# Kernel optimization log

Hardware: AMD Instinct MI355X
Metric: run time of the kernel (lower is better)

## Reference

```python
import jax, jax.numpy as jnp
import numpy as np

EPS = 1e-12  # F.normalize eps


def _gather_nb(var, idx):
    # var: [B, N, C], idx: [B, N, K] -> [B, N, K, C]; out[b,n,k,c] = var[b, idx[b,n,k], c]
    return jnp.take_along_axis(var[:, :, None, :], idx[:, :, :, None], axis=1)


def _l2norm(v):
    n = jnp.sqrt(jnp.sum(v * v, axis=-1, keepdims=True))
    return v / jnp.maximum(n, EPS)


def setup_inputs() -> dict:
    key = jax.random.key(0)
    ks = jax.random.split(key, 16)
    B, N, K, dim, hid = 4, 4096, 16, 128, 64
    s = 0.05
    return {
        "pos": jax.random.normal(ks[0], (B, N, 3), jnp.float32),
        "x": jax.random.normal(ks[1], (B, dim, N), jnp.float32),
        "idx": jax.random.randint(ks[2], (B, N, K), 0, N, jnp.int64),
        "dist": jax.random.uniform(ks[3], (B, N, K), jnp.float32),
        "W_qkv": jax.random.normal(ks[4], (3 * dim, dim), jnp.float32) * s,
        "W1": jax.random.normal(ks[5], (hid, 10), jnp.float32) * s,
        "b1": jax.random.normal(ks[6], (hid,), jnp.float32) * s,
        "W2": jax.random.normal(ks[7], (dim, hid), jnp.float32) * s,
        "b2": jax.random.normal(ks[8], (dim,), jnp.float32) * s,
        "Wm1": jax.random.normal(ks[9], (4 * dim, dim), jnp.float32) * s,
        "bm1": jax.random.normal(ks[10], (4 * dim,), jnp.float32) * s,
        "Wm2": jax.random.normal(ks[11], (dim, 4 * dim), jnp.float32) * s,
        "bm2": jax.random.normal(ks[12], (dim,), jnp.float32) * s,
    }


def reference(pos, x, idx, dist, W_qkv, W1, b1, W2, b2, Wm1, bm1, Wm2, bm2):
    B, _, N = x.shape
    xt = jnp.transpose(x, (0, 2, 1))                      # [B, N, C]
    qkv = xt @ W_qkv.T                                    # [B, N, 3C]
    Q, K_, V = jnp.split(qkv, 3, axis=-1)

    Qg = _gather_nb(Q, idx)                               # [B, N, K, C]
    Kg = _gather_nb(K_, idx)
    Vg = _gather_nb(V, idx)

    # position embedding: [center(3) | neighbor(3) | diff(3) | dist(1)] -> MLP 10->hid->C
    pos_nb = _gather_nb(pos, idx)                         # [B, N, K, 3]
    pos_c = jnp.broadcast_to(pos[:, :, None, :], pos_nb.shape)
    feat10 = jnp.concatenate(
        [pos_c, pos_nb, pos_c - pos_nb, dist[..., None]], axis=-1)  # [B, N, K, 10]
    pos_emb = jax.nn.relu(feat10 @ W1.T + b1) @ W2.T + b2  # [B, N, K, C]

    Knorm = _l2norm(Kg + pos_emb)                         # [B, N, K, C]
    Vrel = jax.nn.relu(Vg + pos_emb)                      # [B, N, K, C]
    Qn = _l2norm(Qg)                                      # [B, N, K, C]

    # kv_context: contract over N per neighbor slot k -> [B, K, C, C]
    kv = jnp.einsum('bnkc,bnkd->bkcd', Knorm, Vrel)
    # (1/N) Qn @ kv, then sum over k -> [B, N, C]
    agg = jnp.einsum('bnkc,bkcd->bnd', Qn, kv) / N

    out = jax.nn.relu(agg @ Wm1.T + bm1) @ Wm2.T + bm2 + xt  # [B, N, C]
    return jnp.transpose(out, (0, 2, 1))                     # [B, C, N]
```

## Files before the change

kernel.cpp:

```cpp
#include <hip/hip_runtime.h>
#include <math.h>

#define Bn 4
#define Nn 4096
#define Kn 16
#define Cn 128
#define HIDn 64

#define OFF_WQKVBF 0
#define OFF_WM1BF  24576
#define OFF_WM2BF  57344
#define OFF_W2BFG  90112
#define OFF_QNBF   94208
#define OFF_KMBF   1142784
#define OFF_VMBF   2191360
#define OFF_KVT32  3239936
#define OFF_KVTBF  4288512
#define OFF_AGG0   4812800
#define OFF_AGG1   6909952
#define OFF_FLAG   9007104

typedef short bf16x8 __attribute__((ext_vector_type(8)));
typedef float f32x4 __attribute__((ext_vector_type(4)));

__device__ inline unsigned short f2bf(float f) {
  union { float f; unsigned u; } v; v.f = f;
  unsigned r = v.u + 0x7fffu + ((v.u >> 16) & 1u);
  return (unsigned short)(r >> 16);
}
__device__ inline float b2f(unsigned short s) {
  union { unsigned u; float f; } v; v.u = ((unsigned)s) << 16; return v.f;
}

__global__ void k0_prep(const float* __restrict__ Wqkv,
                        const float* __restrict__ Wm1, const float* __restrict__ Wm2,
                        const float* __restrict__ W2,
                        const int* __restrict__ idx_raw, float* ws) {
  if (blockIdx.x == 0 && threadIdx.x == 0) {
    int any = 0;
    for (int i = 0; i < 64; ++i) any |= idx_raw[2 * i + 1];
    ((int*)(ws + OFF_FLAG))[0] = (any == 0) ? 1 : 0;
  }
  int t = blockIdx.x * 256 + threadIdx.x;
  if (t < 49152) { ((unsigned short*)(ws + OFF_WQKVBF))[t] = f2bf(Wqkv[t]); return; }
  t -= 49152;
  if (t < 65536) { ((unsigned short*)(ws + OFF_WM1BF))[t] = f2bf(Wm1[t]); return; }
  t -= 65536;
  if (t < 65536) { ((unsigned short*)(ws + OFF_WM2BF))[t] = f2bf(Wm2[t]); return; }
  t -= 65536;
  if (t < 8192) { ((unsigned short*)(ws + OFF_W2BFG))[t] = f2bf(W2[t]); return; }
}

__global__ __launch_bounds__(256, 2) void k1_qkv(const float* __restrict__ x, float* ws) {
  __shared__ __align__(16) unsigned short a_lds[32 * 136];
  __shared__ __align__(16) float qkv_lds[32 * 388];
  const unsigned short* Wq = (const unsigned short*)(ws + OFF_WQKVBF);
  unsigned short* Qnbf = (unsigned short*)(ws + OFF_QNBF);
  unsigned short* KmBF = (unsigned short*)(ws + OFF_KMBF);
  unsigned short* VmBF = (unsigned short*)(ws + OFF_VMBF);
  int b = blockIdx.x >> 7;
  int n0 = (blockIdx.x & 127) << 5;
  int t = threadIdx.x;
  int w = t >> 6, l = t & 63, ml = l & 15, gq = l >> 4;
#pragma unroll
  for (int i = 0; i < 16; ++i) {
    int id = t + 256 * i;
    int c = id >> 5, j = id & 31;
    a_lds[j * 136 + c] = f2bf(x[(b * Cn + c) * Nn + n0 + j]);
  }
  __syncthreads();
  f32x4 acc[2][6];
#pragma unroll
  for (int i = 0; i < 2; ++i)
#pragma unroll
    for (int j = 0; j < 6; ++j) acc[i][j] = (f32x4)0.f;
#pragma unroll
  for (int kc = 0; kc < 4; ++kc) {
    bf16x8 av0 = *(const bf16x8*)&a_lds[ml * 136 + kc * 32 + 8 * gq];
    bf16x8 av1 = *(const bf16x8*)&a_lds[(ml + 16) * 136 + kc * 32 + 8 * gq];
#pragma unroll
    for (int nf = 0; nf < 6; ++nf) {
      int m = 96 * w + 16 * nf + ml;
      bf16x8 bv = *(const bf16x8*)&Wq[m * 128 + kc * 32 + 8 * gq];
      acc[0][nf] = __builtin_amdgcn_mfma_f32_16x16x32_bf16(av0, bv, acc[0][nf], 0, 0, 0);
      acc[1][nf] = __builtin_amdgcn_mfma_f32_16x16x32_bf16(av1, bv, acc[1][nf], 0, 0, 0);
    }
  }
#pragma unroll
  for (int mf = 0; mf < 2; ++mf)
#pragma unroll
    for (int nf = 0; nf < 6; ++nf)
#pragma unroll
      for (int r = 0; r < 4; ++r)
        qkv_lds[(16 * mf + 4 * gq + r) * 388 + 96 * w + 16 * nf + ml] = acc[mf][nf][r];
  __syncthreads();
  {
    int g = t >> 3, l8 = t & 7;
    float4 q4[4];
    float ss = 0.f;
#pragma unroll
    for (int q = 0; q < 4; ++q) {
      q4[q] = *(const float4*)&qkv_lds[g * 388 + l8 * 16 + 4 * q];
      ss = fmaf(q4[q].x, q4[q].x, ss); ss = fmaf(q4[q].y, q4[q].y, ss);
      ss = fmaf(q4[q].z, q4[q].z, ss); ss = fmaf(q4[q].w, q4[q].w, ss);
    }
    ss += __shfl_xor(ss, 1); ss += __shfl_xor(ss, 2); ss += __shfl_xor(ss, 4);
    float sc = 1.f / fmaxf(sqrtf(ss), 1e-12f);
    union { unsigned short us[8]; uint4 u4; } o0, o1;
#pragma unroll
    for (int q = 0; q < 2; ++q) {
      o0.us[q * 4 + 0] = f2bf(q4[q].x * sc); o0.us[q * 4 + 1] = f2bf(q4[q].y * sc);
      o0.us[q * 4 + 2] = f2bf(q4[q].z * sc); o0.us[q * 4 + 3] = f2bf(q4[q].w * sc);
    }
#pragma unroll
    for (int q = 0; q < 2; ++q) {
      o1.us[q * 4 + 0] = f2bf(q4[2 + q].x * sc); o1.us[q * 4 + 1] = f2bf(q4[2 + q].y * sc);
      o1.us[q * 4 + 2] = f2bf(q4[2 + q].z * sc); o1.us[q * 4 + 3] = f2bf(q4[2 + q].w * sc);
    }
    *(uint4*)&Qnbf[(b * Nn + n0 + g) * Cn + l8 * 16] = o0.u4;
    *(uint4*)&Qnbf[(b * Nn + n0 + g) * Cn + l8 * 16 + 8] = o1.u4;
  }
#pragma unroll
  for (int i = 0; i < 2; ++i) {
    int id = t + 256 * i;
    int row = id >> 4, c8 = id & 15;
    const float* kp = &qkv_lds[row * 388 + 128 + c8 * 8];
    const float* vp = &qkv_lds[row * 388 + 256 + c8 * 8];
    union { unsigned short us[8]; uint4 u4; } ko, vo;
#pragma unroll
    for (int j = 0; j < 8; ++j) { ko.us[j] = f2bf(kp[j]); vo.us[j] = f2bf(vp[j]); }
    *(uint4*)&KmBF[(b * Nn + n0 + row) * Cn + c8 * 8] = ko.u4;
    *(uint4*)&VmBF[(b * Nn + n0 + row) * Cn + c8 * 8] = vo.u4;
  }
}

#define CH2 8
__global__ __launch_bounds__(256, 2) void k2_kv(const float* __restrict__ pos,
                                                const float* __restrict__ dist,
                                                const int* __restrict__ idxp,
                                                const float* __restrict__ W1,
                                                const float* __restrict__ b1,
                                                const float* __restrict__ b2,
                                                float* ws) {
  __shared__ __align__(16) unsigned short h_lds[32 * 72];
  __shared__ float pe_lds[32 * 132];
  __shared__ __align__(16) unsigned short KnT[128 * 40];
  __shared__ __align__(16) unsigned short VrT[128 * 40];
  __shared__ float W1s[640];
  __shared__ float b1s[64];
  __shared__ float b2s[128];
  __shared__ int jn_s[32];

  const unsigned short* KmBF = (const unsigned short*)(ws + OFF_KMBF);
  const unsigned short* VmBF = (const unsigned short*)(ws + OFF_VMBF);
  const unsigned short* W2g = (const unsigned short*)(ws + OFF_W2BFG);
  float* kvt = ws + OFF_KVT32;
  int flag = ((const int*)(ws + OFF_FLAG))[0];

  int bid = blockIdx.x;
  int b = bid & 3;
  int rest = bid >> 2;
  int k = rest & 15, ch = rest >> 4;
  int t = threadIdx.x;
  int w = t >> 6, l = t & 63;
  int ml = l & 15, gq = l >> 4;

  for (int i = t; i < 640; i += 256) W1s[i] = W1[i];
  if (t < 64) b1s[t] = b1[t];
  if (t < 128) b2s[t] = b2[t];

  f32x4 acc[2][8];
#pragma unroll
  for (int i = 0; i < 2; ++i)
#pragma unroll
    for (int j = 0; j < 8; ++j) acc[i][j] = (f32x4)0.f;

  int g = t >> 3, l8 = t & 7;

  for (int it = 0; it < 16; ++it) {
    int n0 = ch * 512 + it * 32;
    __syncthreads();
    {
      int n = n0 + g;
      int fidx = (b * Nn + n) * Kn + k;
      int jn = flag ? idxp[2 * fidx] : idxp[fidx];
      if (l8 == 0) jn_s[g] = jn;
      float dd = dist[fidx];
      float pc0 = pos[(b * Nn + n) * 3 + 0], pc1 = pos[(b * Nn + n) * 3 + 1], pc2 = pos[(b * Nn + n) * 3 + 2];
      float pn0 = pos[(b * Nn + jn) * 3 + 0], pn1 = pos[(b * Nn + jn) * 3 + 1], pn2 = pos[(b * Nn + jn) * 3 + 2];
      float f10[10] = {pc0, pc1, pc2, pn0, pn1, pn2, pc0 - pn0, pc1 - pn1, pc2 - pn2, dd};
      union { unsigned short us[8]; uint4 u4; } hv;
#pragma unroll
      for (int oo = 0; oo < 8; ++oo) {
        int o = l8 * 8 + oo;
        float a = b1s[o];
#pragma unroll
        for (int i2 = 0; i2 < 10; ++i2) a = fmaf(W1s[o * 10 + i2], f10[i2], a);
        hv.us[oo] = f2bf(fmaxf(a, 0.f));
      }
      *(uint4*)&h_lds[g * 72 + l8 * 8] = hv.u4;
    }
    __syncthreads();
    {
      f32x4 pacc[2][2];
#pragma unroll
      for (int i = 0; i < 2; ++i)
#pragma unroll
        for (int j = 0; j < 2; ++j) pacc[i][j] = (f32x4)0.f;
#pragma unroll
      for (int hc = 0; hc < 64; hc += 32) {
        bf16x8 av[2];
#pragma unroll
        for (int mf = 0; mf < 2; ++mf)
          av[mf] = *(const bf16x8*)&h_lds[(ml + 16 * mf) * 72 + hc + 8 * gq];
#pragma unroll
        for (int nf = 0; nf < 2; ++nf) {
          int c = 32 * w + 16 * nf + ml;
          bf16x8 bv = *(const bf16x8*)&W2g[c * 64 + hc + 8 * gq];
          pacc[0][nf] = __builtin_amdgcn_mfma_f32_16x16x32_bf16(av[0], bv, pacc[0][nf], 0, 0, 0);
          pacc[1][nf] = __builtin_amdgcn_mfma_f32_16x16x32_bf16(av[1], bv, pacc[1][nf], 0, 0, 0);
        }
      }
#pragma unroll
      for (int mf = 0; mf < 2; ++mf)
#pragma unroll
        for (int nf = 0; nf < 2; ++nf) {
          int c = 32 * w + 16 * nf + ml;
          float b2v = b2s[c];
#pragma unroll
          for (int r = 0; r < 4; ++r)
            pe_lds[(16 * mf + 4 * gq + r) * 132 + c] = pacc[mf][nf][r] + b2v;
        }
    }
    __syncthreads();
    {
      int jn = jn_s[g];
      const unsigned short* krow = &KmBF[(b * Nn + jn) * Cn];
      const unsigned short* vrow = &VmBF[(b * Nn + jn) * Cn];
      union { unsigned short us[8]; uint4 u4; } ka, kb, va, vb;
      ka.u4 = *(const uint4*)&krow[l8 * 16];
      kb.u4 = *(const uint4*)&krow[l8 * 16 + 8];
      va.u4 = *(const uint4*)&vrow[l8 * 16];
      vb.u4 = *(const uint4*)&vrow[l8 * 16 + 8];
      float kr[16], vr[16];
      float ss = 0.f;
#pragma unroll
      for (int q = 0; q < 4; ++q) {
        float4 p = *(const float4*)&pe_lds[g * 132 + l8 * 16 + 4 * q];
        float pv[4] = {p.x, p.y, p.z, p.w};
#pragma unroll
        for (int j2 = 0; j2 < 4; ++j2) {
          int j = 4 * q + j2;
          unsigned short ku = (j < 8) ? ka.us[j] : kb.us[j - 8];
          unsigned short vu = (j < 8) ? va.us[j] : vb.us[j - 8];
          kr[j] = b2f(ku) + pv[j2];
          vr[j] = fmaxf(b2f(vu) + pv[j2], 0.f);
          ss = fmaf(kr[j], kr[j], ss);
        }
      }
      ss += __shfl_xor(ss, 1); ss += __shfl_xor(ss, 2); ss += __shfl_xor(ss, 4);
      float sc = 1.f / fmaxf(sqrtf(ss), 1e-12f);
#pragma unroll
      for (int j = 0; j < 16; ++j) {
        int c = l8 * 16 + j;
        int sw = g ^ (((c >> 4) & 3) << 3);
        KnT[c * 40 + sw] = f2bf(kr[j] * sc);
        VrT[c * 40 + sw] = f2bf(vr[j]);
      }
    }
    __syncthreads();
    {
      bf16x8 av[2];
#pragma unroll
      for (int mf = 0; mf < 2; ++mf) {
        int d = 32 * w + 16 * mf + ml;
        av[mf] = *(const bf16x8*)&VrT[d * 40 + (8 * gq ^ ((((d >> 4) & 3)) << 3))];
      }
#pragma unroll
      for (int nf = 0; nf < 8; ++nf) {
        int c = 16 * nf + ml;
        bf16x8 bv = *(const bf16x8*)&KnT[c * 40 + (8 * gq ^ ((((c >> 4) & 3)) << 3))];
#pragma unroll
        for (int mf = 0; mf < 2; ++mf)
          acc[mf][nf] = __builtin_amdgcn_mfma_f32_16x16x32_bf16(av[mf], bv, acc[mf][nf], 0, 0, 0);
      }
    }
  }
  float* kvp = kvt + (b * Kn + k) * Cn * Cn;
#pragma unroll
  for (int mf = 0; mf < 2; ++mf)
#pragma unroll
    for (int nf = 0; nf < 8; ++nf) {
      int c = 16 * nf + ml;
#pragma unroll
      for (int r = 0; r < 4; ++r) {
        int d = 32 * w + 16 * mf + 4 * gq + r;
        atomicAdd(&kvp[d * Cn + c], acc[mf][nf][r]);
      }
    }
}

__global__ __launch_bounds__(256) void k2b_cvt(float* ws) {
  const float* src = ws + OFF_KVT32;
  unsigned short* dst = (unsigned short*)(ws + OFF_KVTBF);
  int i = blockIdx.x * 256 + threadIdx.x;
  float4 a = *(const float4*)&src[i * 8];
  float4 c = *(const float4*)&src[i * 8 + 4];
  union { unsigned short us[8]; uint4 u4; } o;
  o.us[0] = f2bf(a.x); o.us[1] = f2bf(a.y); o.us[2] = f2bf(a.z); o.us[3] = f2bf(a.w);
  o.us[4] = f2bf(c.x); o.us[5] = f2bf(c.y); o.us[6] = f2bf(c.z); o.us[7] = f2bf(c.w);
  *(uint4*)&dst[i * 8] = o.u4;
}

__global__ __launch_bounds__(256, 4) void k3_agg(const int* __restrict__ idxp, float* ws) {
  __shared__ __align__(16) unsigned short qt[32 * 136];
  const unsigned short* Qnbf = (const unsigned short*)(ws + OFF_QNBF);
  const unsigned short* kvtbf = (const unsigned short*)(ws + OFF_KVTBF);
  int flag = ((const int*)(ws + OFF_FLAG))[0];

  int bid = blockIdx.x;
  int b = bid & 3;
  int kh = (bid >> 2) & 1;
  int nt = bid >> 3;
  int n0 = nt * 32;
  int t = threadIdx.x;
  int w = t >> 6, l = t & 63;
  int ml = l & 15, gq = l >> 4;

  f32x4 acc[2][2];
#pragma unroll
  for (int i = 0; i < 2; ++i)
#pragma unroll
    for (int j = 0; j < 2; ++j) acc[i][j] = (f32x4)0.f;

  for (int kk = 0; kk < 8; ++kk) {
    int k = kh * 8 + kk;
    __syncthreads();
#pragma unroll
    for (int i = 0; i < 2; ++i) {
      int id = t + 256 * i;
      int row = id >> 4, c16 = id & 15;
      int fidx = (b * Nn + n0 + row) * Kn + k;
      int jn = flag ? idxp[2 * fidx] : idxp[fidx];
      uint4 v = *(const uint4*)&Qnbf[(b * Nn + jn) * Cn + c16 * 8];
      *(uint4*)&qt[row * 136 + c16 * 8] = v;
    }
    __syncthreads();
    const unsigned short* kvp = &kvtbf[(b * Kn + k) * Cn * Cn];
#pragma unroll
    for (int c0 = 0; c0 < 128; c0 += 32) {
      bf16x8 a0 = *(const bf16x8*)&qt[ml * 136 + c0 + 8 * gq];
      bf16x8 a1 = *(const bf16x8*)&qt[(ml + 16) * 136 + c0 + 8 * gq];
#pragma unroll
      for (int nf = 0; nf < 2; ++nf) {
        int d = 32 * w + 16 * nf + ml;
        bf16x8 bv = *(const bf16x8*)&kvp[d * Cn + c0 + 8 * gq];
        acc[0][nf] = __builtin_amdgcn_mfma_f32_16x16x32_bf16(a0, bv, acc[0][nf], 0, 0, 0);
        acc[1][nf] = __builtin_amdgcn_mfma_f32_16x16x32_bf16(a1, bv, acc[1][nf], 0, 0, 0);
      }
    }
  }
  float* ag = ws + (kh ? OFF_AGG1 : OFF_AGG0);
#pragma unroll
  for (int mf = 0; mf < 2; ++mf)
#pragma unroll
    for (int nf = 0; nf < 2; ++nf) {
      int d = 32 * w + 16 * nf + ml;
#pragma unroll
      for (int r = 0; r < 4; ++r) {
        int n = n0 + 16 * mf + 4 * gq + r;
        ag[(b * Nn + n) * Cn + d] = acc[mf][nf][r];
      }
    }
}

__global__ __launch_bounds__(256, 2) void k4_mlp(const float* __restrict__ x,
                                                 const float* __restrict__ bm1,
                                                 const float* __restrict__ bm2,
                                                 float* __restrict__ out, float* ws) {
  __shared__ __align__(16) unsigned short a_lds[32 * 136];
  __shared__ __align__(16) unsigned short h_lds[32 * 520];
  __shared__ float out_s[128 * 33];
  const float* agg0 = ws + OFF_AGG0;
  const float* agg1 = ws + OFF_AGG1;
  const unsigned short* Wm1bf = (const unsigned short*)(ws + OFF_WM1BF);
  const unsigned short* Wm2bf = (const unsigned short*)(ws + OFF_WM2BF);
  const float invN = 1.f / (float)Nn;
  int b = blockIdx.x >> 7;
  int n0 = (blockIdx.x & 127) << 5;
  int t = threadIdx.x;
  int w = t >> 6, l = t & 63, ml = l & 15, gq = l >> 4;
#pragma unroll
  for (int i = 0; i < 4; ++i) {
    int id = t + 256 * i;
    int row = id >> 5, c4 = id & 31;
    int off = (b * Nn + n0 + row) * Cn + c4 * 4;
    float4 v0 = *(const float4*)&agg0[off];
    float4 v1 = *(const float4*)&agg1[off];
    union { unsigned short us[4]; uint2 u2; } o;
    o.us[0] = f2bf((v0.x + v1.x) * invN); o.us[1] = f2bf((v0.y + v1.y) * invN);
    o.us[2] = f2bf((v0.z + v1.z) * invN); o.us[3] = f2bf((v0.w + v1.w) * invN);
    *(uint2*)&a_lds[row * 136 + c4 * 4] = o.u2;
  }
  __syncthreads();
  {
    f32x4 hacc[2][8];
#pragma unroll
    for (int i = 0; i < 2; ++i)
#pragma unroll
      for (int j = 0; j < 8; ++j) hacc[i][j] = (f32x4)0.f;
#pragma unroll
    for (int kc = 0; kc < 4; ++kc) {
      bf16x8 av0 = *(const bf16x8*)&a_lds[ml * 136 + kc * 32 + 8 * gq];
      bf16x8 av1 = *(const bf16x8*)&a_lds[(ml + 16) * 136 + kc * 32 + 8 * gq];
#pragma unroll
      for (int nf = 0; nf < 8; ++nf) {
        int h = 128 * w + 16 * nf + ml;
        bf16x8 bv = *(const bf16x8*)&Wm1bf[h * 128 + kc * 32 + 8 * gq];
        hacc[0][nf] = __builtin_amdgcn_mfma_f32_16x16x32_bf16(av0, bv, hacc[0][nf], 0, 0, 0);
        hacc[1][nf] = __builtin_amdgcn_mfma_f32_16x16x32_bf16(av1, bv, hacc[1][nf], 0, 0, 0);
      }
    }
#pragma unroll
    for (int mf = 0; mf < 2; ++mf)
#pragma unroll
      for (int nf = 0; nf < 8; ++nf) {
        int h = 128 * w + 16 * nf + ml;
        float bias = bm1[h];
#pragma unroll
        for (int r = 0; r < 4; ++r)
          h_lds[(16 * mf + 4 * gq + r) * 520 + h] = f2bf(fmaxf(hacc[mf][nf][r] + bias, 0.f));
      }
  }
  __syncthreads();
  {
    f32x4 oacc[2][2];
#pragma unroll
    for (int i = 0; i < 2; ++i)
#pragma unroll
      for (int j = 0; j < 2; ++j) oacc[i][j] = (f32x4)0.f;
#pragma unroll
    for (int kc = 0; kc < 16; ++kc) {
      bf16x8 av0 = *(const bf16x8*)&h_lds[ml * 520 + kc * 32 + 8 * gq];
      bf16x8 av1 = *(const bf16x8*)&h_lds[(ml + 16) * 520 + kc * 32 + 8 * gq];
#pragma unroll
      for (int nf = 0; nf < 2; ++nf) {
        int co = 32 * w + 16 * nf + ml;
        bf16x8 bv = *(const bf16x8*)&Wm2bf[co * 512 + kc * 32 + 8 * gq];
        oacc[0][nf] = __builtin_amdgcn_mfma_f32_16x16x32_bf16(av0, bv, oacc[0][nf], 0, 0, 0);
        oacc[1][nf] = __builtin_amdgcn_mfma_f32_16x16x32_bf16(av1, bv, oacc[1][nf], 0, 0, 0);
      }
    }
#pragma unroll
    for (int mf = 0; mf < 2; ++mf)
#pragma unroll
      for (int nf = 0; nf < 2; ++nf) {
        int co = 32 * w + 16 * nf + ml;
        float bias = bm2[co];
#pragma unroll
        for (int r = 0; r < 4; ++r)
          out_s[co * 33 + 16 * mf + 4 * gq + r] = oacc[mf][nf][r] + bias;
      }
  }
  __syncthreads();
#pragma unroll
  for (int i = 0; i < 16; ++i) {
    int id = t + 256 * i;
    int co = id >> 5, j = id & 31;
    out[(b * Cn + co) * Nn + n0 + j] = out_s[co * 33 + j] + x[(b * Cn + co) * Nn + n0 + j];
  }
}

extern "C" void kernel_launch(void* const* d_in, const int* in_sizes, int n_in,
                              void* d_out, int out_size, void* d_ws, size_t ws_size,
                              hipStream_t stream) {
  const float* pos  = (const float*)d_in[0];
  const float* x    = (const float*)d_in[1];
  const int*   idx  = (const int*)d_in[2];
  const float* dist = (const float*)d_in[3];
  const float* Wqkv = (const float*)d_in[4];
  const float* W1   = (const float*)d_in[5];
  const float* b1   = (const float*)d_in[6];
  const float* W2   = (const float*)d_in[7];
  const float* b2   = (const float*)d_in[8];
  const float* Wm1  = (const float*)d_in[9];
  const float* bm1  = (const float*)d_in[10];
  const float* Wm2  = (const float*)d_in[11];
  const float* bm2  = (const float*)d_in[12];
  float* out = (float*)d_out;
  float* ws = (float*)d_ws;

  hipMemsetAsync(ws + OFF_KVT32, 0, (size_t)Bn * Kn * Cn * Cn * sizeof(float), stream);
  hipLaunchKernelGGL(k0_prep, dim3(736), dim3(256), 0, stream, Wqkv, Wm1, Wm2, W2, idx, ws);
  hipLaunchKernelGGL(k1_qkv, dim3(Bn * 128), dim3(256), 0, stream, x, ws);
  hipLaunchKernelGGL(k2_kv, dim3(Bn * Kn * CH2), dim3(256), 0, stream, pos, dist, idx, W1, b1, b2, ws);
  hipLaunchKernelGGL(k2b_cvt, dim3(512), dim3(256), 0, stream, ws);
  hipLaunchKernelGGL(k3_agg, dim3(Bn * 2 * 128), dim3(256), 0, stream, idx, ws);
  hipLaunchKernelGGL(k4_mlp, dim3(Bn * 128), dim3(256), 0, stream, x, bm1, bm2, out, ws);
}
```

Before: 177.2 us.

## Prefetch neighbor K/V rows early and transpose via row-major LDS staging

The gathered K/V bf16 rows are now loaded from global memory in the first phase, right after the neighbor index is read, so their latency overlaps the position-MLP work instead of waiting behind a shared-memory index broadcast. The transposed K/V tiles are built in two steps: each thread first writes its normalized row into a padded row-major LDS buffer with 16-byte stores, then, after an extra barrier, every thread packs one column into 16-byte stores of the transposed buffer. This replaces the scattered 2-byte swizzled transpose writes. The cost is extra LDS, an extra barrier per iteration, more live registers across phases, and possible bank conflicts on the column reads.

```diff
diff --git a/kernel.cpp b/kernel.cpp
--- a/kernel.cpp
+++ b/kernel.cpp
@@ -144,12 +144,13 @@
                                                 float* ws) {
   __shared__ __align__(16) unsigned short h_lds[32 * 72];
   __shared__ float pe_lds[32 * 132];
+  __shared__ __align__(16) unsigned short K_rm[32 * 136];
+  __shared__ __align__(16) unsigned short V_rm[32 * 136];
   __shared__ __align__(16) unsigned short KnT[128 * 40];
   __shared__ __align__(16) unsigned short VrT[128 * 40];
   __shared__ float W1s[640];
   __shared__ float b1s[64];
   __shared__ float b2s[128];
-  __shared__ int jn_s[32];
 
   const unsigned short* KmBF = (const unsigned short*)(ws + OFF_KMBF);
   const unsigned short* VmBF = (const unsigned short*)(ws + OFF_VMBF);
@@ -176,15 +177,23 @@
     for (int j = 0; j < 8; ++j) acc[i][j] = (f32x4)0.f;
 
   int g = t >> 3, l8 = t & 7;
+  int side = t >> 7, cc = t & 127;
+
+  __syncthreads();
 
   for (int it = 0; it < 16; ++it) {
     int n0 = ch * 512 + it * 32;
-    __syncthreads();
+    union { unsigned short us[8]; uint4 u4; } ka, kb, va, vb;
     {
       int n = n0 + g;
       int fidx = (b * Nn + n) * Kn + k;
       int jn = flag ? idxp[2 * fidx] : idxp[fidx];
-      if (l8 == 0) jn_s[g] = jn;
+      const unsigned short* krow = &KmBF[(b * Nn + jn) * Cn];
+      const unsigned short* vrow = &VmBF[(b * Nn + jn) * Cn];
+      ka.u4 = *(const uint4*)&krow[l8 * 16];
+      kb.u4 = *(const uint4*)&krow[l8 * 16 + 8];
+      va.u4 = *(const uint4*)&vrow[l8 * 16];
+      vb.u4 = *(const uint4*)&vrow[l8 * 16 + 8];
       float dd = dist[fidx];
       float pc0 = pos[(b * Nn + n) * 3 + 0], pc1 = pos[(b * Nn + n) * 3 + 1], pc2 = pos[(b * Nn + n) * 3 + 2];
       float pn0 = pos[(b * Nn + jn) * 3 + 0], pn1 = pos[(b * Nn + jn) * 3 + 1], pn2 = pos[(b * Nn + jn) * 3 + 2];
@@ -234,14 +243,6 @@
     }
     __syncthreads();
     {
-      int jn = jn_s[g];
-      const unsigned short* krow = &KmBF[(b * Nn + jn) * Cn];
-      const unsigned short* vrow = &VmBF[(b * Nn + jn) * Cn];
-      union { unsigned short us[8]; uint4 u4; } ka, kb, va, vb;
-      ka.u4 = *(const uint4*)&krow[l8 * 16];
-      kb.u4 = *(const uint4*)&krow[l8 * 16 + 8];
-      va.u4 = *(const uint4*)&vrow[l8 * 16];
-      vb.u4 = *(const uint4*)&vrow[l8 * 16 + 8];
       float kr[16], vr[16];
       float ss = 0.f;
 #pragma unroll
@@ -260,26 +261,46 @@
       }
       ss += __shfl_xor(ss, 1); ss += __shfl_xor(ss, 2); ss += __shfl_xor(ss, 4);
       float sc = 1.f / fmaxf(sqrtf(ss), 1e-12f);
-#pragma unroll
-      for (int j = 0; j < 16; ++j) {
-        int c = l8 * 16 + j;
-        int sw = g ^ (((c >> 4) & 3) << 3);
-        KnT[c * 40 + sw] = f2bf(kr[j] * sc);
-        VrT[c * 40 + sw] = f2bf(vr[j]);
+      union { unsigned short us[8]; uint4 u4; } o;
+#pragma unroll
+      for (int half = 0; half < 2; ++half) {
+#pragma unroll
+        for (int j = 0; j < 8; ++j) o.us[j] = f2bf(kr[half * 8 + j] * sc);
+        *(uint4*)&K_rm[g * 136 + l8 * 16 + half * 8] = o.u4;
+      }
+#pragma unroll
+      for (int half = 0; half < 2; ++half) {
+#pragma unroll
+        for (int j = 0; j < 8; ++j) o.us[j] = f2bf(vr[half * 8 + j]);
+        *(uint4*)&V_rm[g * 136 + l8 * 16 + half * 8] = o.u4;
+      }
+    }
+    __syncthreads();
+    {
+      const unsigned short* src = side ? V_rm : K_rm;
+      unsigned short* dst = side ? VrT : KnT;
+      unsigned v[16];
+#pragma unroll
+      for (int i = 0; i < 16; ++i) {
+        unsigned lo = src[(2 * i) * 136 + cc];
+        unsigned hi = src[(2 * i + 1) * 136 + cc];
+        v[i] = lo | (hi << 16);
+      }
+#pragma unroll
+      for (int i = 0; i < 4; ++i) {
+        uint4 pk = {v[4 * i], v[4 * i + 1], v[4 * i + 2], v[4 * i + 3]};
+        *(uint4*)&dst[cc * 40 + 8 * i] = pk;
       }
     }
     __syncthreads();
     {
       bf16x8 av[2];
 #pragma unroll
-      for (int mf = 0; mf < 2; ++mf) {
-        int d = 32 * w + 16 * mf + ml;
-        av[mf] = *(const bf16x8*)&VrT[d * 40 + (8 * gq ^ ((((d >> 4) & 3)) << 3))];
-      }
+      for (int mf = 0; mf < 2; ++mf)
+        av[mf] = *(const bf16x8*)&VrT[(32 * w + 16 * mf + ml) * 40 + 8 * gq];
 #pragma unroll
       for (int nf = 0; nf < 8; ++nf) {
-        int c = 16 * nf + ml;
-        bf16x8 bv = *(const bf16x8*)&KnT[c * 40 + (8 * gq ^ ((((c >> 4) & 3)) << 3))];
+        bf16x8 bv = *(const bf16x8*)&KnT[(16 * nf + ml) * 40 + 8 * gq];
 #pragma unroll
         for (int mf = 0; mf < 2; ++mf)
           acc[mf][nf] = __builtin_amdgcn_mfma_f32_16x16x32_bf16(av[mf], bv, acc[mf][nf], 0, 0, 0);
```

Result: no change. 179.9 us (+1.5%).
